# Kernel optimization log

Hardware: AMD Instinct MI355X
Metric: run time of the kernel (lower is better)

Reference implementation:

```python
import jax, jax.numpy as jnp
import numpy as np

N_NODES = 100000
N_EDGES = 3200000
N_FEAT = 128
DIM = 256
N_CLASSES = 16
BN_EPS = 1e-5


def _glorot(key, shape):
    fan_in, fan_out = shape[0], shape[1]
    lim = float(np.sqrt(6.0 / (fan_in + fan_out)))
    return jax.random.uniform(key, shape, jnp.float32, -lim, lim)


def setup_inputs() -> dict:
    key = jax.random.key(0)
    ks = jax.random.split(key, 16)
    x = jax.random.normal(ks[0], (N_NODES, N_FEAT), jnp.float32)
    edge_index = jax.random.randint(ks[1], (2, N_EDGES), 0, N_NODES, jnp.int64)
    inp = {"x": x, "edge_index": edge_index}
    # conv1 MLP: num_features -> dim -> dim
    inp["w1a"] = _glorot(ks[2], (N_FEAT, DIM)); inp["b1a"] = jnp.zeros((DIM,), jnp.float32)
    inp["w1b"] = _glorot(ks[3], (DIM, DIM));    inp["b1b"] = jnp.zeros((DIM,), jnp.float32)
    inp["g1"] = jnp.ones((DIM,), jnp.float32);  inp["be1"] = jnp.zeros((DIM,), jnp.float32)
    # conv2 MLP
    inp["w2a"] = _glorot(ks[4], (DIM, DIM)); inp["b2a"] = jnp.zeros((DIM,), jnp.float32)
    inp["w2b"] = _glorot(ks[5], (DIM, DIM)); inp["b2b"] = jnp.zeros((DIM,), jnp.float32)
    inp["g2"] = jnp.ones((DIM,), jnp.float32); inp["be2"] = jnp.zeros((DIM,), jnp.float32)
    # conv3 MLP
    inp["w3a"] = _glorot(ks[6], (DIM, DIM)); inp["b3a"] = jnp.zeros((DIM,), jnp.float32)
    inp["w3b"] = _glorot(ks[7], (DIM, DIM)); inp["b3b"] = jnp.zeros((DIM,), jnp.float32)
    # fc2: dim -> num_classes
    inp["wfc"] = _glorot(ks[8], (DIM, N_CLASSES)); inp["bfc"] = jnp.zeros((N_CLASSES,), jnp.float32)
    return inp


def _gin_conv(h, src, dst, wa, ba, wb, bb):
    # sum-aggregate neighbor features: agg[i] = sum_{(j->i)} h[j]; eps=0 so root weight = 1
    agg = jax.ops.segment_sum(h[src], dst, num_segments=N_NODES)
    z = jax.nn.relu((h + agg) @ wa + ba)
    return z @ wb + bb


def _batchnorm(h, gamma, beta):
    # training-mode BN over node dim (biased variance, as torch forward)
    m = h.mean(axis=0)
    v = ((h - m) ** 2).mean(axis=0)
    return gamma * (h - m) / jnp.sqrt(v + BN_EPS) + beta


def reference(x, edge_index, w1a, b1a, w1b, b1b, g1, be1,
              w2a, b2a, w2b, b2b, g2, be2,
              w3a, b3a, w3b, b3b, wfc, bfc):
    src, dst = edge_index[0], edge_index[1]
    h = jax.nn.relu(_gin_conv(x, src, dst, w1a, b1a, w1b, b1b))
    h = _batchnorm(h, g1, be1)
    h = jax.nn.relu(_gin_conv(h, src, dst, w2a, b2a, w2b, b2b))
    h = _batchnorm(h, g2, be2)
    h = jax.nn.relu(_gin_conv(h, src, dst, w3a, b3a, w3b, b3b))
    # dropout p=0.5 is identity in eval mode
    logits = h @ wfc + bfc
    return jax.nn.log_softmax(logits, axis=-1)
```

## Files before the change

kernel.cpp:

```cpp
#include <hip/hip_runtime.h>

typedef unsigned int  u32;
typedef unsigned short u16;

#define NND 100000
#define MPAD 100096
#define NE  3200000
#define F0  128
#define DIM 256
#define NC  16

#define BSH   9
#define NBUCK 196
#define CAP   18432
#define EPB   8192

typedef __bf16 bf16x8 __attribute__((ext_vector_type(8)));
typedef float  f32x4  __attribute__((ext_vector_type(4)));

__device__ __forceinline__ float b2f(u16 h){ return __uint_as_float(((u32)h)<<16); }
__device__ __forceinline__ u16 f2b(float f){
    u32 u = __float_as_uint(f);
    return (u16)((u + 0x7fffu + ((u>>16)&1u)) >> 16);
}
__device__ __forceinline__ float lo16(u32 u){ return __uint_as_float(u<<16); }
__device__ __forceinline__ float hi16(u32 u){ return __uint_as_float(u & 0xffff0000u); }

__global__ void probe_kernel(const u32* __restrict__ xw, const int* __restrict__ ei,
                             int* __restrict__ mode, int* __restrict__ gcur,
                             float* __restrict__ stats){
    int t = threadIdx.x;
    if(t < NBUCK) gcur[t] = 0;
    #pragma unroll
    for(int i=0;i<4;i++) stats[t + 256*i] = 0.f;
    if(t==0){
        int insane = 0;
        for(int i=0;i<64;i++){
            u32 w  = xw[i];
            u32 lo = w & 0xffffu;
            u32 e  = (lo >> 7) & 0xff;
            if(lo != 0 && (e < 48 || e > 208)) insane++;
        }
        mode[0] = (insane > 8) ? 1 : 0;
        int zeros = 0;
        for(int i=0;i<16;i++) if(ei[2*i+1]==0) zeros++;
        mode[1] = (zeros==16) ? 1 : 0;
    }
}

__device__ __forceinline__ int ld_src(const int* ei, int i64f, long e){
    return i64f ? ei[2*e] : ei[e];
}
__device__ __forceinline__ int ld_dst(const int* ei, int i64f, long e){
    return i64f ? ei[2*((long)NE + e)] : ei[(long)NE + e];
}

__global__ __launch_bounds__(256) void bucketA(const int* __restrict__ ei,
        const int* __restrict__ mode, u32* __restrict__ bucketArr,
        int* __restrict__ gcur){
    __shared__ u32 stag[EPB];
    __shared__ u16 sbuck[EPB];
    __shared__ int cnt[NBUCK];
    __shared__ int ofs[NBUCK];
    __shared__ int wofs[NBUCK];
    __shared__ int gbase[NBUCK];
    __shared__ int ps[256];
    int tid = threadIdx.x;
    int i64f = mode[1];
    long e0 = (long)blockIdx.x * EPB;
    int n = (int)min((long)EPB, (long)NE - e0);
    if(tid < NBUCK) cnt[tid] = 0;
    __syncthreads();
    for(int i=tid;i<n;i+=256){
        int d = ld_dst(ei, i64f, e0+i);
        atomicAdd(&cnt[d>>BSH], 1);
    }
    __syncthreads();
    ps[tid] = (tid < NBUCK) ? cnt[tid] : 0;
    __syncthreads();
    for(int o=1;o<256;o<<=1){
        int v = (tid>=o) ? ps[tid-o] : 0;
        __syncthreads();
        ps[tid] += v;
        __syncthreads();
    }
    if(tid < NBUCK){
        int ex = ps[tid] - cnt[tid];
        ofs[tid] = ex; wofs[tid] = ex;
        gbase[tid] = cnt[tid] ? atomicAdd(&gcur[tid], cnt[tid]) : 0;
    }
    __syncthreads();
    for(int i=tid;i<n;i+=256){
        int s = ld_src(ei, i64f, e0+i);
        int d = ld_dst(ei, i64f, e0+i);
        int b = d>>BSH;
        int r = atomicAdd(&wofs[b], 1);
        stag[r]  = ((u32)s<<BSH) | (u32)(d & ((1<<BSH)-1));
        sbuck[r] = (u16)b;
    }
    __syncthreads();
    for(int i=tid;i<n;i+=256){
        int b = sbuck[i];
        int pos = gbase[b] + (i - ofs[b]);
        if(pos < CAP) bucketArr[(size_t)b*CAP + pos] = stag[i];
    }
}

__global__ __launch_bounds__(256) void bucketB(const u32* __restrict__ bucketArr,
        const int* __restrict__ gcnt,
        int* __restrict__ rp, int* __restrict__ ssrc){
    __shared__ u32 stag[CAP];
    __shared__ int deg[512];
    __shared__ int lrp[512];
    __shared__ int cur[512];
    __shared__ int ps[256];
    int b = blockIdx.x, tid = threadIdx.x;
    ps[tid] = (tid < NBUCK) ? gcnt[tid] : 0;
    __syncthreads();
    for(int o=1;o<256;o<<=1){
        int v = (tid>=o) ? ps[tid-o] : 0;
        __syncthreads();
        ps[tid] += v;
        __syncthreads();
    }
    int base = (b>0) ? ps[b-1] : 0;
    int n = min(gcnt[b], CAP);
    const u32* ba = bucketArr + (size_t)b*CAP;
    deg[tid] = 0; deg[tid+256] = 0;
    __syncthreads();
    for(int i=tid;i<n;i+=256){
        atomicAdd(&deg[ba[i] & 511], 1);
    }
    __syncthreads();
    ps[tid] = deg[2*tid] + deg[2*tid+1];
    __syncthreads();
    for(int o=1;o<256;o<<=1){
        int v = (tid>=o) ? ps[tid-o] : 0;
        __syncthreads();
        ps[tid] += v;
        __syncthreads();
    }
    {
        int ep = (tid==0) ? 0 : ps[tid-1];
        lrp[2*tid]   = ep;
        lrp[2*tid+1] = ep + deg[2*tid];
        cur[2*tid]   = lrp[2*tid];
        cur[2*tid+1] = lrp[2*tid+1];
    }
    __syncthreads();
    for(int i=tid;i<512;i+=256){
        int node = (b<<BSH) + i;
        if(node <= NND) rp[node] = base + lrp[i];
    }
    for(int i=tid;i<n;i+=256){
        u32 v = ba[i];
        int r = atomicAdd(&cur[v & 511], 1);
        stag[r] = v >> BSH;
    }
    __syncthreads();
    for(int i=tid;i<n;i+=256){
        ssrc[base + i] = (int)stag[i];
    }
}

__global__ void cvt_x(const float* __restrict__ xf, u16* __restrict__ Xc,
                      const int* __restrict__ mode){
    if(!mode[0]) return;
    size_t i = ((size_t)blockIdx.x*256 + threadIdx.x)*8;
    float4 a = *(const float4*)(xf+i);
    float4 b = *(const float4*)(xf+i+4);
    uint4 pk;
    pk.x = (u32)f2b(a.x) | ((u32)f2b(a.y)<<16);
    pk.y = (u32)f2b(a.z) | ((u32)f2b(a.w)<<16);
    pk.z = (u32)f2b(b.x) | ((u32)f2b(b.y)<<16);
    pk.w = (u32)f2b(b.z) | ((u32)f2b(b.w)<<16);
    *(uint4*)(Xc + i) = pk;
}

__device__ __forceinline__ float ldf(const void* p, int i, int f32f){
    return f32f ? ((const float*)p)[i] : b2f(((const u16*)p)[i]);
}
__global__ void merged_cvt(
        const void* w1a, const void* w1b, const void* w2a, const void* w2b,
        const void* w3a, const void* w3b, const void* wfc,
        const void* b1a, const void* b1b, const void* g1, const void* be1,
        const void* b2a, const void* b2b, const void* g2, const void* be2,
        const void* b3a, const void* b3b, const void* bfcp,
        u16* __restrict__ Wt1a, u16* __restrict__ Wt1b, u16* __restrict__ Wt2a,
        u16* __restrict__ Wt2b, u16* __restrict__ Wt3a, u16* __restrict__ Wt3b,
        u16* __restrict__ Wfc, u16* __restrict__ Vc, const int* __restrict__ mode){
    int b = blockIdx.x, t = threadIdx.x;
    int f32f = mode[0];
    if(b < 128){
        int id = b*256 + t;
        int k = id / DIM, n = id % DIM;
        Wt1a[n*F0 + k] = f2b(ldf(w1a, id, f32f));
        return;
    }
    b -= 128;
    if(b < 5*256){
        int wi = b >> 8;
        const void* W = (wi==0)?w1b:(wi==1)?w2a:(wi==2)?w2b:(wi==3)?w3a:w3b;
        u16* Wt = (wi==0)?Wt1b:(wi==1)?Wt2a:(wi==2)?Wt2b:(wi==3)?Wt3a:Wt3b;
        int id = (b & 255)*256 + t;
        int k = id / DIM, n = id % DIM;
        Wt[n*DIM + k] = f2b(ldf(W, id, f32f));
        return;
    }
    b -= 5*256;
    if(b < 16){
        int id = b*256 + t;
        int k = id / NC, c = id % NC;
        Wfc[c*DIM + k] = f2b(ldf(wfc, id, f32f));
        return;
    }
    b -= 16;
    {
        const void* ps[11] = {b1a,b1b,g1,be1,b2a,b2b,g2,be2,b3a,b3b,bfcp};
        int lens[11] = {DIM,DIM,DIM,DIM,DIM,DIM,DIM,DIM,DIM,DIM,NC};
        if(t < lens[b]) Vc[b*256 + t] = f2b(ldf(ps[b], t, f32f));
    }
}

template<int LPI>
__global__ __launch_bounds__(256) void agg2(const u16* __restrict__ hA,
        const u16* __restrict__ hB, const int* __restrict__ mode,
        const int* __restrict__ rp, const int* __restrict__ ssrc,
        u16* __restrict__ out,
        const float* __restrict__ stats, const u16* __restrict__ g,
        const u16* __restrict__ be, int use_bn, int M){
    const int F = LPI*8;
    const int IPW = 64/LPI;
    int node = blockIdx.x*4 + (threadIdx.x>>6);
    if(node >= M) return;
    int lane = threadIdx.x & 63;
    int li   = lane & (LPI-1);
    int slot = lane / LPI;
    const u16* h = (LPI==16 && mode[0]) ? hB : hA;
    const int boff = li*8;

    int e0 = rp[node], e1 = rp[node+1];
    int n_items = e1 - e0 + 1;
    float acc[8] = {0.f,0.f,0.f,0.f,0.f,0.f,0.f,0.f};

    auto item = [&](int i)->int { return (i==0) ? node : ssrc[e0 + i - 1]; };
    auto addu = [&](uint4 u){
        acc[0]+=lo16(u.x); acc[1]+=hi16(u.x);
        acc[2]+=lo16(u.y); acc[3]+=hi16(u.y);
        acc[4]+=lo16(u.z); acc[5]+=hi16(u.z);
        acc[6]+=lo16(u.w); acc[7]+=hi16(u.w);
    };

    int i = 0;
    for(; i + 8*IPW <= n_items; i += 8*IPW){
        int s[8];
        #pragma unroll
        for(int j=0;j<8;j++) s[j] = item(i + j*IPW + slot);
        uint4 u[8];
        #pragma unroll
        for(int j=0;j<8;j++) u[j] = *(const uint4*)(h + (size_t)s[j]*F + boff);
        #pragma unroll
        for(int j=0;j<8;j++) addu(u[j]);
    }
    for(; i + IPW <= n_items; i += IPW){
        int s = item(i + slot);
        addu(*(const uint4*)(h + (size_t)s*F + boff));
    }
    if(i < n_items){
        int r = n_items - i;
        if(slot < r){
            int s = item(i + slot);
            addu(*(const uint4*)(h + (size_t)s*F + boff));
        }
    }

    #pragma unroll
    for(int j=0;j<8;j++){
        if(LPI==16) acc[j] += __shfl_xor(acc[j], 16);
        acc[j] += __shfl_xor(acc[j], 32);
    }

    if(slot == 0){
        float res[8];
        if(use_bn){
            float inv_m = 1.0f / (float)M;
            float cnt = (float)n_items;
            #pragma unroll
            for(int j=0;j<8;j++){
                int f = boff + j;
                float mean = stats[f]*inv_m;
                float var  = fmaxf(stats[F+f]*inv_m - mean*mean, 0.f);
                float rstd = rsqrtf(var + 1e-5f);
                float gg = b2f(g[f]);
                float a = gg*rstd;
                float bb = b2f(be[f]) - a*mean;
                res[j] = a*acc[j] + cnt*bb;
            }
        } else {
            #pragma unroll
            for(int j=0;j<8;j++) res[j] = acc[j];
        }
        uint4 o;
        o.x = (u32)f2b(res[0]) | ((u32)f2b(res[1])<<16);
        o.y = (u32)f2b(res[2]) | ((u32)f2b(res[3])<<16);
        o.z = (u32)f2b(res[4]) | ((u32)f2b(res[5])<<16);
        o.w = (u32)f2b(res[6]) | ((u32)f2b(res[7])<<16);
        *(uint4*)(out + (size_t)node*F + boff) = o;
    }
}

#define FBM 64
#define ZP  264
template<int KA>
__global__ __launch_bounds__(256) void mlp_fused(
        const u16* __restrict__ A, const u16* __restrict__ WaT,
        const u16* __restrict__ ba, const u16* __restrict__ WbT,
        const u16* __restrict__ bb, u16* __restrict__ C,
        float* __restrict__ stats, int do_stats,
        int do_fc, const u16* __restrict__ WfcT, const u16* __restrict__ bfc,
        void* __restrict__ out, const int* __restrict__ mode){
    __shared__ __align__(16) u16 zt[FBM*ZP];
    __shared__ float colS[DIM], colS2[DIM];
    int tid = threadIdx.x;
    int w = tid>>6, lane = tid&63;
    int q = lane>>4, mr = lane&15;
    int m0 = blockIdx.x*FBM;

    if(do_stats){ colS[tid]=0.f; colS2[tid]=0.f; }

    f32x4 acc[4][4];
    #pragma unroll
    for(int i=0;i<4;i++)
        #pragma unroll
        for(int c=0;c<4;c++) acc[i][c] = (f32x4){0.f,0.f,0.f,0.f};

    {
        const int NK = KA/32;
        bf16x8 a0[4], b0[4];
        #pragma unroll
        for(int i=0;i<4;i++)
            a0[i] = *reinterpret_cast<const bf16x8*>(A + (size_t)(m0 + i*16 + mr)*KA + q*8);
        #pragma unroll
        for(int c=0;c<4;c++)
            b0[c] = *reinterpret_cast<const bf16x8*>(WaT + (size_t)(w*64 + c*16 + mr)*KA + q*8);
        #pragma unroll
        for(int k=0;k<NK;k++){
            bf16x8 a1[4], b1[4];
            if(k+1<NK){
                #pragma unroll
                for(int i=0;i<4;i++)
                    a1[i] = *reinterpret_cast<const bf16x8*>(A + (size_t)(m0 + i*16 + mr)*KA + (k+1)*32 + q*8);
                #pragma unroll
                for(int c=0;c<4;c++)
                    b1[c] = *reinterpret_cast<const bf16x8*>(WaT + (size_t)(w*64 + c*16 + mr)*KA + (k+1)*32 + q*8);
            }
            #pragma unroll
            for(int i=0;i<4;i++)
                #pragma unroll
                for(int c=0;c<4;c++)
                    acc[i][c] = __builtin_amdgcn_mfma_f32_16x16x32_bf16(a0[i], b0[c], acc[i][c], 0, 0, 0);
            if(k+1<NK){
                #pragma unroll
                for(int i=0;i<4;i++){ a0[i]=a1[i]; b0[i]=b1[i]; }
            }
        }
    }
    #pragma unroll
    for(int c=0;c<4;c++){
        int col = w*64 + c*16 + mr;
        float bav = b2f(ba[col]);
        #pragma unroll
        for(int i=0;i<4;i++){
            #pragma unroll
            for(int r=0;r<4;r++){
                int row = i*16 + q*4 + r;
                zt[row*ZP + col] = f2b(fmaxf(acc[i][c][r] + bav, 0.f));
            }
            acc[i][c] = (f32x4){0.f,0.f,0.f,0.f};
        }
    }
    __syncthreads();

    {
        const int NK = DIM/32;
        bf16x8 b0[4];
        #pragma unroll
        for(int c=0;c<4;c++)
            b0[c] = *reinterpret_cast<const bf16x8*>(WbT + (size_t)(w*64 + c*16 + mr)*DIM + q*8);
        #pragma unroll
        for(int k=0;k<NK;k++){
            bf16x8 b1[4];
            if(k+1<NK){
                #pragma unroll
                for(int c=0;c<4;c++)
                    b1[c] = *reinterpret_cast<const bf16x8*>(WbT + (size_t)(w*64 + c*16 + mr)*DIM + (k+1)*32 + q*8);
            }
            bf16x8 af[4];
            #pragma unroll
            for(int i=0;i<4;i++)
                af[i] = *reinterpret_cast<const bf16x8*>(&zt[(i*16+mr)*ZP + k*32 + q*8]);
            #pragma unroll
            for(int i=0;i<4;i++)
                #pragma unroll
                for(int c=0;c<4;c++)
                    acc[i][c] = __builtin_amdgcn_mfma_f32_16x16x32_bf16(af[i], b0[c], acc[i][c], 0, 0, 0);
            if(k+1<NK){
                #pragma unroll
                for(int c=0;c<4;c++) b0[c]=b1[c];
            }
        }
    }

    if(!do_fc){
        #pragma unroll
        for(int c=0;c<4;c++){
            int col = w*64 + c*16 + mr;
            float bv = b2f(bb[col]);
            float s = 0.f, s2 = 0.f;
            #pragma unroll
            for(int i=0;i<4;i++){
                int row = m0 + i*16 + q*4;
                #pragma unroll
                for(int r=0;r<4;r++){
                    float v = fmaxf(acc[i][c][r] + bv, 0.f);
                    u16 o = f2b(v);
                    C[(size_t)(row + r)*DIM + col] = o;
                    if(do_stats && (row + r) < NND){
                        float vr = b2f(o);
                        s += vr; s2 += vr*vr;
                    }
                }
            }
            if(do_stats){
                atomicAdd(&colS[col], s);
                atomicAdd(&colS2[col], s2);
            }
        }
        if(do_stats){
            __syncthreads();
            atomicAdd(&stats[tid], colS[tid]);
            atomicAdd(&stats[DIM+tid], colS2[tid]);
        }
    } else {
        __syncthreads();
        #pragma unroll
        for(int c=0;c<4;c++){
            int col = w*64 + c*16 + mr;
            float bv = b2f(bb[col]);
            #pragma unroll
            for(int i=0;i<4;i++)
                #pragma unroll
                for(int r=0;r<4;r++)
                    zt[(i*16 + q*4 + r)*ZP + col] = f2b(fmaxf(acc[i][c][r] + bv, 0.f));
        }
        __syncthreads();
        f32x4 fa = (f32x4){0.f,0.f,0.f,0.f};
        #pragma unroll
        for(int k0=0; k0<DIM; k0+=32){
            bf16x8 za = *reinterpret_cast<const bf16x8*>(&zt[(w*16+mr)*ZP + k0 + q*8]);
            bf16x8 wb = *reinterpret_cast<const bf16x8*>(WfcT + (size_t)mr*DIM + k0 + q*8);
            fa = __builtin_amdgcn_mfma_f32_16x16x32_bf16(za, wb, fa, 0, 0, 0);
        }
        float bv = b2f(bfc[mr]);
        int f32o = mode[0];
        #pragma unroll
        for(int r=0;r<4;r++){
            float val = fa[r] + bv;
            float m = val;
            #pragma unroll
            for(int o=1;o<16;o<<=1) m = fmaxf(m, __shfl_xor(m, o));
            float ex = expf(val - m);
            float s = ex;
            #pragma unroll
            for(int o=1;o<16;o<<=1) s += __shfl_xor(s, o);
            float res = val - m - logf(s);
            int row = m0 + w*16 + q*4 + r;
            if(row < NND){
                if(f32o) ((float*)out)[(size_t)row*NC + mr] = res;
                else     ((u16*)out)[(size_t)row*NC + mr] = f2b(res);
            }
        }
    }
}

extern "C" void kernel_launch(void* const* d_in, const int* in_sizes, int n_in,
                              void* d_out, int out_size, void* d_ws, size_t ws_size,
                              hipStream_t stream){
    const void* x   = d_in[0];
    const int*  ei  = (const int*)d_in[1];
    const void* w1a = d_in[2];  const void* b1a = d_in[3];
    const void* w1b = d_in[4];  const void* b1b = d_in[5];
    const void* g1  = d_in[6];  const void* be1 = d_in[7];
    const void* w2a = d_in[8];  const void* b2a = d_in[9];
    const void* w2b = d_in[10]; const void* b2b = d_in[11];
    const void* g2  = d_in[12]; const void* be2 = d_in[13];
    const void* w3a = d_in[14]; const void* b3a = d_in[15];
    const void* w3b = d_in[16]; const void* b3b = d_in[17];
    const void* wfc = d_in[18]; const void* bfc = d_in[19];

    char* base = (char*)d_ws;
    size_t off = 0;
    auto alloc = [&](size_t bytes)->void*{
        void* p = base + off;
        off = (off + bytes + 255) & ~(size_t)255;
        return p;
    };
    u16*  P     = (u16*)alloc((size_t)MPAD*DIM*2);
    u16*  Q     = (u16*)alloc((size_t)MPAD*DIM*2);
    int*  ssrc  = (int*)alloc((size_t)NE*4);
    u32*  bArr  = (u32*)alloc((size_t)NBUCK*CAP*4);
    int*  gcur  = (int*)alloc((size_t)NBUCK*4);
    int*  rp    = (int*)alloc((size_t)(NND+1)*4);
    float* stats= (float*)alloc(4*DIM*4);
    int*  mode  = (int*)alloc(16);
    u16* Wt1a = (u16*)alloc((size_t)F0*DIM*2);
    u16* Wt1b = (u16*)alloc((size_t)DIM*DIM*2);
    u16* Wt2a = (u16*)alloc((size_t)DIM*DIM*2);
    u16* Wt2b = (u16*)alloc((size_t)DIM*DIM*2);
    u16* Wt3a = (u16*)alloc((size_t)DIM*DIM*2);
    u16* Wt3b = (u16*)alloc((size_t)DIM*DIM*2);
    u16* Vc   = (u16*)alloc(11*256*2);
    u16* Wfc  = (u16*)alloc((size_t)DIM*NC*2);
    u16* Xc   = P;
    float* statsA = stats;
    float* statsB = stats + 2*DIM;

    probe_kernel<<<1, 256, 0, stream>>>((const u32*)x, ei, mode, gcur, stats);

    bucketA<<<(NE + EPB - 1)/EPB, 256, 0, stream>>>(ei, mode, bArr, gcur);
    bucketB<<<NBUCK, 256, 0, stream>>>(bArr, gcur, rp, ssrc);

    cvt_x<<<(NND*F0)/(256*8), 256, 0, stream>>>((const float*)x, Xc, mode);
    merged_cvt<<<128 + 5*256 + 16 + 11, 256, 0, stream>>>(
        w1a,w1b,w2a,w2b,w3a,w3b,wfc, b1a,b1b,g1,be1,b2a,b2b,g2,be2,b3a,b3b,bfc,
        Wt1a,Wt1b,Wt2a,Wt2b,Wt3a,Wt3b,Wfc,Vc, mode);

    int mgrid = MPAD/FBM;

    agg2<16><<<NND/4, 256, 0, stream>>>((const u16*)x, Xc, mode, rp, ssrc, Q,
                                        statsA, Vc, Vc, 0, NND);
    mlp_fused<F0><<<mgrid, 256, 0, stream>>>(Q, Wt1a, Vc+0*256, Wt1b, Vc+1*256, P,
                                             statsA, 1, 0, Wfc, Vc+10*256, d_out, mode);

    agg2<32><<<NND/4, 256, 0, stream>>>(P, P, mode, rp, ssrc, Q,
                                        statsA, Vc+2*256, Vc+3*256, 1, NND);
    mlp_fused<DIM><<<mgrid, 256, 0, stream>>>(Q, Wt2a, Vc+4*256, Wt2b, Vc+5*256, P,
                                              statsB, 1, 0, Wfc, Vc+10*256, d_out, mode);

    agg2<32><<<NND/4, 256, 0, stream>>>(P, P, mode, rp, ssrc, Q,
                                        statsB, Vc+6*256, Vc+7*256, 1, NND);
    mlp_fused<DIM><<<mgrid, 256, 0, stream>>>(Q, Wt3a, Vc+8*256, Wt3b, Vc+9*256, P,
                                              statsA, 0, 1, Wfc, Vc+10*256, d_out, mode);
}
```

Baseline: 1.055 ms.

## Fuse neighbor aggregation into the MLP kernel via shared-memory staging

Each layer's gather-sum aggregation now runs inside the fused MLP kernel. Every 64-row block aggregates its own nodes into shared memory, and the first GEMM reads its A operand from there, so the intermediate aggregated tensor is no longer written to and read back from global memory and three launches go away. In exchange, each block has only 4 waves doing the irregular gather, with a shallower unroll of 4 instead of 8. Occupancy may also be limited by the shared-memory tile, so gather latency hiding may get worse. Buffers are ping-ponged between P and Q to avoid in-place read/write hazards.

```diff
diff --git a/kernel.cpp b/kernel.cpp
--- a/kernel.cpp
+++ b/kernel.cpp
@@ -222,103 +222,21 @@
     }
 }
 
-template<int LPI>
-__global__ __launch_bounds__(256) void agg2(const u16* __restrict__ hA,
-        const u16* __restrict__ hB, const int* __restrict__ mode,
-        const int* __restrict__ rp, const int* __restrict__ ssrc,
-        u16* __restrict__ out,
-        const float* __restrict__ stats, const u16* __restrict__ g,
-        const u16* __restrict__ be, int use_bn, int M){
-    const int F = LPI*8;
-    const int IPW = 64/LPI;
-    int node = blockIdx.x*4 + (threadIdx.x>>6);
-    if(node >= M) return;
-    int lane = threadIdx.x & 63;
-    int li   = lane & (LPI-1);
-    int slot = lane / LPI;
-    const u16* h = (LPI==16 && mode[0]) ? hB : hA;
-    const int boff = li*8;
-
-    int e0 = rp[node], e1 = rp[node+1];
-    int n_items = e1 - e0 + 1;
-    float acc[8] = {0.f,0.f,0.f,0.f,0.f,0.f,0.f,0.f};
-
-    auto item = [&](int i)->int { return (i==0) ? node : ssrc[e0 + i - 1]; };
-    auto addu = [&](uint4 u){
-        acc[0]+=lo16(u.x); acc[1]+=hi16(u.x);
-        acc[2]+=lo16(u.y); acc[3]+=hi16(u.y);
-        acc[4]+=lo16(u.z); acc[5]+=hi16(u.z);
-        acc[6]+=lo16(u.w); acc[7]+=hi16(u.w);
-    };
-
-    int i = 0;
-    for(; i + 8*IPW <= n_items; i += 8*IPW){
-        int s[8];
-        #pragma unroll
-        for(int j=0;j<8;j++) s[j] = item(i + j*IPW + slot);
-        uint4 u[8];
-        #pragma unroll
-        for(int j=0;j<8;j++) u[j] = *(const uint4*)(h + (size_t)s[j]*F + boff);
-        #pragma unroll
-        for(int j=0;j<8;j++) addu(u[j]);
-    }
-    for(; i + IPW <= n_items; i += IPW){
-        int s = item(i + slot);
-        addu(*(const uint4*)(h + (size_t)s*F + boff));
-    }
-    if(i < n_items){
-        int r = n_items - i;
-        if(slot < r){
-            int s = item(i + slot);
-            addu(*(const uint4*)(h + (size_t)s*F + boff));
-        }
-    }
-
-    #pragma unroll
-    for(int j=0;j<8;j++){
-        if(LPI==16) acc[j] += __shfl_xor(acc[j], 16);
-        acc[j] += __shfl_xor(acc[j], 32);
-    }
-
-    if(slot == 0){
-        float res[8];
-        if(use_bn){
-            float inv_m = 1.0f / (float)M;
-            float cnt = (float)n_items;
-            #pragma unroll
-            for(int j=0;j<8;j++){
-                int f = boff + j;
-                float mean = stats[f]*inv_m;
-                float var  = fmaxf(stats[F+f]*inv_m - mean*mean, 0.f);
-                float rstd = rsqrtf(var + 1e-5f);
-                float gg = b2f(g[f]);
-                float a = gg*rstd;
-                float bb = b2f(be[f]) - a*mean;
-                res[j] = a*acc[j] + cnt*bb;
-            }
-        } else {
-            #pragma unroll
-            for(int j=0;j<8;j++) res[j] = acc[j];
-        }
-        uint4 o;
-        o.x = (u32)f2b(res[0]) | ((u32)f2b(res[1])<<16);
-        o.y = (u32)f2b(res[2]) | ((u32)f2b(res[3])<<16);
-        o.z = (u32)f2b(res[4]) | ((u32)f2b(res[5])<<16);
-        o.w = (u32)f2b(res[6]) | ((u32)f2b(res[7])<<16);
-        *(uint4*)(out + (size_t)node*F + boff) = o;
-    }
-}
-
 #define FBM 64
 #define ZP  264
 template<int KA>
-__global__ __launch_bounds__(256) void mlp_fused(
-        const u16* __restrict__ A, const u16* __restrict__ WaT,
-        const u16* __restrict__ ba, const u16* __restrict__ WbT,
-        const u16* __restrict__ bb, u16* __restrict__ C,
-        float* __restrict__ stats, int do_stats,
+__global__ __launch_bounds__(256) void layer_fused(
+        const u16* __restrict__ hA, const u16* __restrict__ hB,
+        const int* __restrict__ mode,
+        const int* __restrict__ rp, const int* __restrict__ ssrc,
+        const float* __restrict__ statsIn, const u16* __restrict__ g,
+        const u16* __restrict__ be, int use_bn,
+        const u16* __restrict__ WaT, const u16* __restrict__ ba,
+        const u16* __restrict__ WbT, const u16* __restrict__ bb,
+        u16* __restrict__ C, float* __restrict__ statsOut, int do_stats,
         int do_fc, const u16* __restrict__ WfcT, const u16* __restrict__ bfc,
-        void* __restrict__ out, const int* __restrict__ mode){
+        void* __restrict__ out){
+    const int AP = KA + 8;
     __shared__ __align__(16) u16 zt[FBM*ZP];
     __shared__ float colS[DIM], colS2[DIM];
     int tid = threadIdx.x;
@@ -328,6 +246,93 @@
 
     if(do_stats){ colS[tid]=0.f; colS2[tid]=0.f; }
 
+    {
+        const int LPI = KA/8;
+        const int IPW = 64/LPI;
+        int li   = lane & (LPI-1);
+        int slot = lane / LPI;
+        int boff = li*8;
+        const u16* h = mode[0] ? hB : hA;
+
+        float aff_a[8], aff_b[8];
+        if(use_bn){
+            float inv_m = 1.0f / (float)NND;
+            #pragma unroll
+            for(int j=0;j<8;j++){
+                int f = boff + j;
+                float mean = statsIn[f]*inv_m;
+                float var  = fmaxf(statsIn[KA+f]*inv_m - mean*mean, 0.f);
+                float rstd = rsqrtf(var + 1e-5f);
+                float gg = b2f(g[f]);
+                aff_a[j] = gg*rstd;
+                aff_b[j] = b2f(be[f]) - aff_a[j]*mean;
+            }
+        } else {
+            #pragma unroll
+            for(int j=0;j<8;j++){ aff_a[j]=1.f; aff_b[j]=0.f; }
+        }
+
+        for(int nl = w; nl < FBM; nl += 4){
+            int node = m0 + nl;
+            float acc[8] = {0.f,0.f,0.f,0.f,0.f,0.f,0.f,0.f};
+            float cnt = 0.f;
+            if(node < NND){
+                int e0 = rp[node], e1 = rp[node+1];
+                int n_items = e1 - e0 + 1;
+                cnt = (float)n_items;
+                auto item = [&](int idx)->int { return (idx==0) ? node : ssrc[e0 + idx - 1]; };
+                auto addu = [&](uint4 u){
+                    acc[0]+=lo16(u.x); acc[1]+=hi16(u.x);
+                    acc[2]+=lo16(u.y); acc[3]+=hi16(u.y);
+                    acc[4]+=lo16(u.z); acc[5]+=hi16(u.z);
+                    acc[6]+=lo16(u.w); acc[7]+=hi16(u.w);
+                };
+                int i = 0;
+                for(; i + 4*IPW <= n_items; i += 4*IPW){
+                    int s0 = item(i + slot);
+                    int s1 = item(i + IPW + slot);
+                    int s2 = item(i + 2*IPW + slot);
+                    int s3 = item(i + 3*IPW + slot);
+                    uint4 u0 = *(const uint4*)(h + (size_t)s0*KA + boff);
+                    uint4 u1 = *(const uint4*)(h + (size_t)s1*KA + boff);
+                    uint4 u2 = *(const uint4*)(h + (size_t)s2*KA + boff);
+                    uint4 u3 = *(const uint4*)(h + (size_t)s3*KA + boff);
+                    addu(u0); addu(u1); addu(u2); addu(u3);
+                }
+                for(; i + IPW <= n_items; i += IPW){
+                    int s = item(i + slot);
+                    addu(*(const uint4*)(h + (size_t)s*KA + boff));
+                }
+                if(i < n_items && slot < n_items - i){
+                    int s = item(i + slot);
+                    addu(*(const uint4*)(h + (size_t)s*KA + boff));
+                }
+            }
+            #pragma unroll
+            for(int j=0;j<8;j++){
+                if(LPI==16) acc[j] += __shfl_xor(acc[j], 16);
+                acc[j] += __shfl_xor(acc[j], 32);
+            }
+            if(slot == 0){
+                uint4 o;
+                float r0 = aff_a[0]*acc[0] + cnt*aff_b[0];
+                float r1 = aff_a[1]*acc[1] + cnt*aff_b[1];
+                float r2 = aff_a[2]*acc[2] + cnt*aff_b[2];
+                float r3 = aff_a[3]*acc[3] + cnt*aff_b[3];
+                float r4 = aff_a[4]*acc[4] + cnt*aff_b[4];
+                float r5 = aff_a[5]*acc[5] + cnt*aff_b[5];
+                float r6 = aff_a[6]*acc[6] + cnt*aff_b[6];
+                float r7 = aff_a[7]*acc[7] + cnt*aff_b[7];
+                o.x = (u32)f2b(r0) | ((u32)f2b(r1)<<16);
+                o.y = (u32)f2b(r2) | ((u32)f2b(r3)<<16);
+                o.z = (u32)f2b(r4) | ((u32)f2b(r5)<<16);
+                o.w = (u32)f2b(r6) | ((u32)f2b(r7)<<16);
+                *(uint4*)(&zt[nl*AP + boff]) = o;
+            }
+        }
+    }
+    __syncthreads();
+
     f32x4 acc[4][4];
     #pragma unroll
     for(int i=0;i<4;i++)
@@ -336,35 +341,35 @@
 
     {
         const int NK = KA/32;
-        bf16x8 a0[4], b0[4];
-        #pragma unroll
-        for(int i=0;i<4;i++)
-            a0[i] = *reinterpret_cast<const bf16x8*>(A + (size_t)(m0 + i*16 + mr)*KA + q*8);
+        bf16x8 b0[4];
         #pragma unroll
         for(int c=0;c<4;c++)
             b0[c] = *reinterpret_cast<const bf16x8*>(WaT + (size_t)(w*64 + c*16 + mr)*KA + q*8);
         #pragma unroll
         for(int k=0;k<NK;k++){
-            bf16x8 a1[4], b1[4];
+            bf16x8 b1[4];
             if(k+1<NK){
-                #pragma unroll
-                for(int i=0;i<4;i++)
-                    a1[i] = *reinterpret_cast<const bf16x8*>(A + (size_t)(m0 + i*16 + mr)*KA + (k+1)*32 + q*8);
                 #pragma unroll
                 for(int c=0;c<4;c++)
                     b1[c] = *reinterpret_cast<const bf16x8*>(WaT + (size_t)(w*64 + c*16 + mr)*KA + (k+1)*32 + q*8);
             }
+            bf16x8 af[4];
             #pragma unroll
             for(int i=0;i<4;i++)
+                af[i] = *reinterpret_cast<const bf16x8*>(&zt[(i*16+mr)*AP + k*32 + q*8]);
+            #pragma unroll
+            for(int i=0;i<4;i++)
                 #pragma unroll
                 for(int c=0;c<4;c++)
-                    acc[i][c] = __builtin_amdgcn_mfma_f32_16x16x32_bf16(a0[i], b0[c], acc[i][c], 0, 0, 0);
+                    acc[i][c] = __builtin_amdgcn_mfma_f32_16x16x32_bf16(af[i], b0[c], acc[i][c], 0, 0, 0);
             if(k+1<NK){
                 #pragma unroll
-                for(int i=0;i<4;i++){ a0[i]=a1[i]; b0[i]=b1[i]; }
-            }
-        }
-    }
+                for(int c=0;c<4;c++) b0[c]=b1[c];
+            }
+        }
+    }
+    __syncthreads();
+
     #pragma unroll
     for(int c=0;c<4;c++){
         int col = w*64 + c*16 + mr;
@@ -438,8 +443,8 @@
         }
         if(do_stats){
             __syncthreads();
-            atomicAdd(&stats[tid], colS[tid]);
-            atomicAdd(&stats[DIM+tid], colS2[tid]);
+            atomicAdd(&statsOut[tid], colS[tid]);
+            atomicAdd(&statsOut[DIM+tid], colS2[tid]);
         }
     } else {
         __syncthreads();
@@ -521,7 +526,7 @@
     u16* Wt3b = (u16*)alloc((size_t)DIM*DIM*2);
     u16* Vc   = (u16*)alloc(11*256*2);
     u16* Wfc  = (u16*)alloc((size_t)DIM*NC*2);
-    u16* Xc   = P;
+    u16* Xc   = Q;
     float* statsA = stats;
     float* statsB = stats + 2*DIM;
 
@@ -537,18 +542,21 @@
 
     int mgrid = MPAD/FBM;
 
-    agg2<16><<<NND/4, 256, 0, stream>>>((const u16*)x, Xc, mode, rp, ssrc, Q,
-                                        statsA, Vc, Vc, 0, NND);
-    mlp_fused<F0><<<mgrid, 256, 0, stream>>>(Q, Wt1a, Vc+0*256, Wt1b, Vc+1*256, P,
-                                             statsA, 1, 0, Wfc, Vc+10*256, d_out, mode);
-
-    agg2<32><<<NND/4, 256, 0, stream>>>(P, P, mode, rp, ssrc, Q,
-                                        statsA, Vc+2*256, Vc+3*256, 1, NND);
-    mlp_fused<DIM><<<mgrid, 256, 0, stream>>>(Q, Wt2a, Vc+4*256, Wt2b, Vc+5*256, P,
-                                              statsB, 1, 0, Wfc, Vc+10*256, d_out, mode);
-
-    agg2<32><<<NND/4, 256, 0, stream>>>(P, P, mode, rp, ssrc, Q,
-                                        statsB, Vc+6*256, Vc+7*256, 1, NND);
-    mlp_fused<DIM><<<mgrid, 256, 0, stream>>>(Q, Wt3a, Vc+8*256, Wt3b, Vc+9*256, P,
-                                              statsA, 0, 1, Wfc, Vc+10*256, d_out, mode);
-}
+    layer_fused<F0><<<mgrid, 256, 0, stream>>>(
+        (const u16*)x, Xc, mode, rp, ssrc,
+        statsA, Vc, Vc, 0,
+        Wt1a, Vc+0*256, Wt1b, Vc+1*256,
+        P, statsA, 1, 0, Wfc, Vc+10*256, d_out);
+
+    layer_fused<DIM><<<mgrid, 256, 0, stream>>>(
+        P, P, mode, rp, ssrc,
+        statsA, Vc+2*256, Vc+3*256, 1,
+        Wt2a, Vc+4*256, Wt2b, Vc+5*256,
+        Q, statsB, 1, 0, Wfc, Vc+10*256, d_out);
+
+    layer_fused<DIM><<<mgrid, 256, 0, stream>>>(
+        Q, Q, mode, rp, ssrc,
+        statsB, Vc+6*256, Vc+7*256, 1,
+        Wt3a, Vc+8*256, Wt3b, Vc+9*256,
+        P, statsA, 0, 1, Wfc, Vc+10*256, d_out);
+}
```

Result: slower. 1.374 ms (+30.2%).
